# Kernel optimization log

Measured on AMD Instinct MI355X. Metric: run time of the kernel, lower is better.

The kernel has to match this reference:

```python
import jax, jax.numpy as jnp
import numpy as np

STEP_SIZE = 0.3333
MAX_STEPS = 8          # >= ceil(max(2*sigma)/step); extra iterations have k==0 (no-op)
TANGENT_DIRECTION = True


def _bilinear_sample(img, p):
    # img: [B,C,H,W], p: [B,2,H,W] normalized coords in [0,1] (x=width, y=height)
    B, C, H, W = img.shape
    fx = p[:, 0] * W - 0.5   # [B,H,W] pixel-center convention
    fy = p[:, 1] * H - 0.5
    x0 = jnp.floor(fx)
    y0 = jnp.floor(fy)
    wx = (fx - x0)[:, None]  # [B,1,H,W]
    wy = (fy - y0)[:, None]
    x0i = jnp.clip(x0.astype(jnp.int32), 0, W - 1)
    x1i = jnp.clip(x0i + 1, 0, W - 1)
    y0i = jnp.clip(y0.astype(jnp.int32), 0, H - 1)
    y1i = jnp.clip(y0i + 1, 0, H - 1)
    gather = jax.vmap(lambda im, yi, xi: im[:, yi, xi])  # per-batch gather -> [B,C,H,W]
    v00 = gather(img, y0i, x0i)
    v01 = gather(img, y0i, x1i)
    v10 = gather(img, y1i, x0i)
    v11 = gather(img, y1i, x1i)
    return (v00 * (1 - wx) + v01 * wx) * (1 - wy) + (v10 * (1 - wx) + v11 * wx) * wy


def _p_start(H, W, dtype):
    xs = (jnp.arange(W, dtype=dtype) + 0.5) / W
    ys = (jnp.arange(H, dtype=dtype) + 0.5) / H
    px = jnp.broadcast_to(xs[None, :], (H, W))
    py = jnp.broadcast_to(ys[:, None], (H, W))
    return jnp.stack([px, py])[None]  # [1,2,H,W]


def _perp(t):
    return jnp.concatenate([t[:, 1:2], -t[:, 0:1]], axis=1)


def _forward(x, tangent, sigma):
    B, C, H, W = x.shape
    dt = x.dtype
    factor = min(H, W) / 1024.0          # input_size_factor relative to 1024 base res
    sigma = sigma * factor               # [B,1,1,1]
    half_width = 2.0 * sigma
    two_sigma2 = 2.0 * sigma * sigma
    step = jnp.asarray(1.0 / (STEP_SIZE * factor), dtype=dt)
    tex = jnp.array([W, H], dtype=dt).reshape(1, 2, 1, 1)
    p0 = _p_start(H, W, dt)

    def one_pass(direction):
        v = direction if TANGENT_DIRECTION else _perp(direction)
        p = p0 + v / tex
        r = jnp.broadcast_to(step, (B, 1, 1, 1))
        c = jnp.zeros_like(x)
        s = jnp.zeros((B, 1, H, W), dt)

        def body(carry, _):
            c, s, v, p, r = carry
            k = jnp.exp(-r * r / two_sigma2)                 # [B,1,1,1]
            k = jnp.where(r < half_width, k, 0.0)
            inb = ((p[:, 0:1] >= 0.0) & (p[:, 0:1] < 1.0) &
                   (p[:, 1:2] >= 0.0) & (p[:, 1:2] < 1.0))   # [B,1,H,W]
            k = jnp.where(inb, k, 0.0)                        # [B,1,H,W]
            c = c + _bilinear_sample(x, p) * k
            s = s + k
            tf = _bilinear_sample(tangent, p)                 # [B,2,H,W]
            if not TANGENT_DIRECTION:
                tf = _perp(tf)
            vt = jnp.sum(v * tf, axis=1, keepdims=True)
            tf = jnp.where(vt < 0.0, -tf, tf)                 # keep marching direction coherent
            return (c, s, tf, p + tf / tex, r + step), None

        (c, s, _, _, _), _ = jax.lax.scan(body, (c, s, v, p, r), None, length=MAX_STEPS)
        return c, s

    c1, s1 = one_pass(tangent)
    c2, s2 = one_pass(-tangent)
    return (x + c1 + c2) / (1.0 + s1 + s2)


def setup_inputs() -> dict:
    key = jax.random.key(0)
    k1, k2, k3 = jax.random.split(key, 3)
    B, C, H, W = 2, 3, 1024, 1024
    x = jax.random.uniform(k1, (B, C, H, W), dtype=jnp.float32)
    t = jax.random.normal(k2, (B, 2, H, W), dtype=jnp.float32)
    t = t / (jnp.sqrt(jnp.sum(t * t, axis=1, keepdims=True)) + 1e-6)  # unit tangent field
    sigma = 2.0 + 4.0 * jax.random.uniform(k3, (B, 1, 1, 1), dtype=jnp.float32)
    return {"x": x, "tangent": t, "sigma": sigma}


def reference(x, tangent, sigma):
    return _forward(x, tangent, sigma)
```

## Files before the change

### kernel.cpp

```cpp
#include <hip/hip_runtime.h>


#define HH 1024
#define WW 1024
#define CC 3
#define BB 2
#define NPIX (HH * WW)

#define TSX 16
#define TSY 16
#define HALO_LO 4
#define NWIN 25

__device__ __forceinline__ unsigned bf16rn(float f) {
    unsigned u = __float_as_uint(f);
    return (u + 0x7fffu + ((u >> 16) & 1u)) >> 16;
}
__device__ __forceinline__ float bf_lo(unsigned u) { return __uint_as_float(u << 16); }
__device__ __forceinline__ float bf_hi(unsigned u) { return __uint_as_float(u & 0xffff0000u); }
__device__ __forceinline__ float uaf(unsigned u)   { return __uint_as_float(u); }

__global__ __launch_bounds__(256) void flow_smooth_lds(
    const float* __restrict__ x, const float* __restrict__ tng,
    const float* __restrict__ sigma, float* __restrict__ out)
{
    __shared__ uint4 win[NWIN * NWIN];

    const int id  = (int)blockIdx.x + ((int)blockIdx.y << 6) + ((int)blockIdx.z << 12);
    const int swz = ((id & 7) << 10) + (id >> 3);
    const int bx = swz & 63;
    const int by = (swz >> 6) & 63;
    const int b  = swz >> 12;

    const int tile_x0 = bx * TSX;
    const int tile_y0 = by * TSY;
    const int win_x0 = tile_x0 - HALO_LO;
    const int win_y0 = tile_y0 - HALO_LO;
    const bool border = (bx == 0) | (bx == 63) | (by == 0) | (by == 63);

    const float* __restrict__ xb  = x   + (size_t)b * CC * NPIX;
    const float* __restrict__ tbx = tng + (size_t)b * 2 * NPIX;
    const float* __restrict__ tby = tbx + NPIX;

    if (!border) {
        const int gbase = win_y0 * WW + win_x0;
        for (unsigned j = threadIdx.x; j < NWIN * NWIN; j += 256) {
            const int jy = (int)(j / NWIN);
            const int jx = (int)j - jy * NWIN;
            const int g = gbase + (jy << 10) + jx;
            uint4 rec;
            rec.x = __float_as_uint(tbx[g]);
            rec.y = __float_as_uint(tby[g]);
            rec.z = bf16rn(xb[g]) | (bf16rn(xb[NPIX + g]) << 16);
            rec.w = bf16rn(xb[2 * NPIX + g]);
            win[j] = rec;
        }
    } else {
        for (unsigned j = threadIdx.x; j < NWIN * NWIN; j += 256) {
            const int jy = (int)(j / NWIN);
            const int jx = (int)j - jy * NWIN;
            const int gy = min(max(win_y0 + jy, 0), HH - 1);
            const int gx = min(max(win_x0 + jx, 0), WW - 1);
            const int g = gy * WW + gx;
            uint4 rec;
            rec.x = __float_as_uint(tbx[g]);
            rec.y = __float_as_uint(tby[g]);
            rec.z = bf16rn(xb[g]) | (bf16rn(xb[NPIX + g]) << 16);
            rec.w = bf16rn(xb[2 * NPIX + g]);
            win[j] = rec;
        }
    }
    __syncthreads();

    const int tx = threadIdx.x & (TSX - 1);
    const int ty = threadIdx.x >> 4;
    const int ix = tile_x0 + tx;
    const int iy = tile_y0 + ty;
    const int pix = iy * WW + ix;

    const float sig = sigma[b];
    const float half_width = 2.0f * sig;
    const float inv2s2 = 1.0f / (2.0f * sig * sig);
    const float step = (float)(1.0 / 0.3333);

    const float r0 = step;
    const float r1 = r0 + step;
    const float r2 = r1 + step;
    const int nlive = (int)(r0 < half_width) + (int)(r1 < half_width) + (int)(r2 < half_width);
    float kk[3];
    kk[0] = __expf(-r0 * r0 * inv2s2);
    kk[1] = __expf(-r1 * r1 * inv2s2);
    kk[2] = __expf(-r2 * r2 * inv2s2);

    const float xc0 = xb[pix];
    const float xc1 = xb[NPIX + pix];
    const float xc2 = xb[2 * NPIX + pix];
    const int cidx = (ty + HALO_LO) * NWIN + (tx + HALO_LO);
    const uint2 qc = *reinterpret_cast<const uint2*>(&win[cidx]);
    const float t0x = uaf(qc.x);
    const float t0y = uaf(qc.y);

    const float invW = 1.0f / WW;
    const float invH = 1.0f / HH;

    float acc0 = 0.f, acc1 = 0.f, acc2 = 0.f, accs = 0.f;

    float vx[2], vy[2], px[2], py[2];
    vx[0] = t0x;  vy[0] = t0y;
    vx[1] = -t0x; vy[1] = -t0y;
    const float p0x = ((float)ix + 0.5f) * invW;
    const float p0y = ((float)iy + 0.5f) * invH;
    px[0] = p0x + vx[0] * invW;  py[0] = p0y + vy[0] * invH;
    px[1] = p0x + vx[1] * invW;  py[1] = p0y + vy[1] * invH;

    if (!border) {
        const int winoff = win_y0 * NWIN + win_x0;
        #pragma unroll
        for (int it = 0; it < 3; ++it) {
            if (it >= nlive) break;
            const float k = kk[it];
            #pragma unroll
            for (int c = 0; c < 2; ++c) {
                const float fx = fmaf(px[c], (float)WW, -0.5f);
                const float fy = fmaf(py[c], (float)HH, -0.5f);
                const float x0f = floorf(fx);
                const float y0f = floorf(fy);
                const float wx = fx - x0f;
                const float wy = fy - y0f;
                const int idx = (int)y0f * NWIN + (int)x0f - winoff;

                const uint4 q00 = win[idx];
                const uint4 q01 = win[idx + 1];
                const uint4 q10 = win[idx + NWIN];
                const uint4 q11 = win[idx + NWIN + 1];

                const float wxm = 1.f - wx, wym = 1.f - wy;
                const float w00 = wxm * wym, w01 = wx * wym;
                const float w10 = wxm * wy,  w11 = wx * wy;

                float tfx = uaf(q00.x) * w00 + uaf(q01.x) * w01
                          + uaf(q10.x) * w10 + uaf(q11.x) * w11;
                float tfy = uaf(q00.y) * w00 + uaf(q01.y) * w01
                          + uaf(q10.y) * w10 + uaf(q11.y) * w11;

                const float k00 = k * w00, k01 = k * w01;
                const float k10 = k * w10, k11 = k * w11;
                acc0 += bf_lo(q00.z) * k00 + bf_lo(q01.z) * k01
                      + bf_lo(q10.z) * k10 + bf_lo(q11.z) * k11;
                acc1 += bf_hi(q00.z) * k00 + bf_hi(q01.z) * k01
                      + bf_hi(q10.z) * k10 + bf_hi(q11.z) * k11;
                acc2 += bf_lo(q00.w) * k00 + bf_lo(q01.w) * k01
                      + bf_lo(q10.w) * k10 + bf_lo(q11.w) * k11;

                const float vt = vx[c] * tfx + vy[c] * tfy;
                const unsigned sgn = __float_as_uint(vt) & 0x80000000u;
                tfx = __uint_as_float(__float_as_uint(tfx) ^ sgn);
                tfy = __uint_as_float(__float_as_uint(tfy) ^ sgn);
                vx[c] = tfx; vy[c] = tfy;
                px[c] += tfx * invW;
                py[c] += tfy * invH;
            }
        }
        float ks = 0.f;
        if (nlive > 0) ks += kk[0];
        if (nlive > 1) ks += kk[1];
        if (nlive > 2) ks += kk[2];
        accs = 2.0f * ks;
    } else {
        #pragma unroll
        for (int it = 0; it < 3; ++it) {
            if (it >= nlive) break;
            const float k = kk[it];
            #pragma unroll
            for (int c = 0; c < 2; ++c) {
                const float fx = fmaf(px[c], (float)WW, -0.5f);
                const float fy = fmaf(py[c], (float)HH, -0.5f);
                const float x0f = floorf(fx);
                const float y0f = floorf(fy);
                const float wx = fx - x0f;
                const float wy = fy - y0f;
                int x0i = (int)x0f;
                int y0i = (int)y0f;
                x0i = min(max(x0i, 0), WW - 1);
                y0i = min(max(y0i, 0), HH - 1);
                const int x1i = min(x0i + 1, WW - 1);
                const int y1i = min(y0i + 1, HH - 1);

                const int jx0 = x0i - win_x0;
                const int jx1 = x1i - win_x0;
                const int jy0 = y0i - win_y0;
                const int jy1 = y1i - win_y0;

                const uint4 q00 = win[jy0 * NWIN + jx0];
                const uint4 q01 = win[jy0 * NWIN + jx1];
                const uint4 q10 = win[jy1 * NWIN + jx0];
                const uint4 q11 = win[jy1 * NWIN + jx1];

                const float wxm = 1.f - wx, wym = 1.f - wy;
                const float w00 = wxm * wym, w01 = wx * wym;
                const float w10 = wxm * wy,  w11 = wx * wy;

                float tfx = uaf(q00.x) * w00 + uaf(q01.x) * w01
                          + uaf(q10.x) * w10 + uaf(q11.x) * w11;
                float tfy = uaf(q00.y) * w00 + uaf(q01.y) * w01
                          + uaf(q10.y) * w10 + uaf(q11.y) * w11;

                const bool inb = (px[c] >= 0.f) & (px[c] < 1.f) &
                                 (py[c] >= 0.f) & (py[c] < 1.f);
                const float kg = inb ? k : 0.f;
                const float k00 = kg * w00, k01 = kg * w01;
                const float k10 = kg * w10, k11 = kg * w11;
                acc0 += bf_lo(q00.z) * k00 + bf_lo(q01.z) * k01
                      + bf_lo(q10.z) * k10 + bf_lo(q11.z) * k11;
                acc1 += bf_hi(q00.z) * k00 + bf_hi(q01.z) * k01
                      + bf_hi(q10.z) * k10 + bf_hi(q11.z) * k11;
                acc2 += bf_lo(q00.w) * k00 + bf_lo(q01.w) * k01
                      + bf_lo(q10.w) * k10 + bf_lo(q11.w) * k11;
                accs += kg;

                const float vt = vx[c] * tfx + vy[c] * tfy;
                const unsigned sgn = __float_as_uint(vt) & 0x80000000u;
                tfx = __uint_as_float(__float_as_uint(tfx) ^ sgn);
                tfy = __uint_as_float(__float_as_uint(tfy) ^ sgn);
                vx[c] = tfx; vy[c] = tfy;
                px[c] += tfx * invW;
                py[c] += tfy * invH;
            }
        }
    }

    const float inv_den = 1.0f / (1.0f + accs);
    float* ob = out + (size_t)b * CC * NPIX;
    ob[pix]            = (xc0 + acc0) * inv_den;
    ob[NPIX + pix]     = (xc1 + acc1) * inv_den;
    ob[2 * NPIX + pix] = (xc2 + acc2) * inv_den;
}

extern "C" void kernel_launch(void* const* d_in, const int* in_sizes, int n_in,
                              void* d_out, int out_size, void* d_ws, size_t ws_size,
                              hipStream_t stream) {
    const float* x  = (const float*)d_in[0];
    const float* t  = (const float*)d_in[1];
    const float* sg = (const float*)d_in[2];
    float* out = (float*)d_out;

    dim3 grid(WW / TSX, HH / TSY, BB);
    flow_smooth_lds<<<grid, dim3(256), 0, stream>>>(x, t, sg, out);
}
```

Measured before the change: 114.7 us.

## Split LDS window into tangent and fp16 color arrays, use packed half FMA

Splits the single 16-byte LDS record into a float2 tangent array and an 8-byte fp16 color array. Color interpolation now runs with packed half2 FMAs instead of bf16 unpacking and scalar FMAs. The tangent sample on the last live iteration is skipped, since its result is never used. Packed half arithmetic for the weighted sums adds rounding error compared to fp32 accumulation, and splitting the arrays means more LDS load instructions per tap.

```diff
diff --git a/kernel.cpp b/kernel.cpp
--- a/kernel.cpp
+++ b/kernel.cpp
@@ -1,4 +1,5 @@
 #include <hip/hip_runtime.h>
+#include <hip/hip_fp16.h>
 
 
 #define HH 1024
@@ -12,19 +13,17 @@
 #define HALO_LO 4
 #define NWIN 25
 
-__device__ __forceinline__ unsigned bf16rn(float f) {
-    unsigned u = __float_as_uint(f);
-    return (u + 0x7fffu + ((u >> 16) & 1u)) >> 16;
+__device__ __forceinline__ float uaf(unsigned u) { return __uint_as_float(u); }
+__device__ __forceinline__ __half2 h2(unsigned u) {
+    __half2 r; *(unsigned*)&r = u; return r;
 }
-__device__ __forceinline__ float bf_lo(unsigned u) { return __uint_as_float(u << 16); }
-__device__ __forceinline__ float bf_hi(unsigned u) { return __uint_as_float(u & 0xffff0000u); }
-__device__ __forceinline__ float uaf(unsigned u)   { return __uint_as_float(u); }
 
 __global__ __launch_bounds__(256) void flow_smooth_lds(
     const float* __restrict__ x, const float* __restrict__ tng,
     const float* __restrict__ sigma, float* __restrict__ out)
 {
-    __shared__ uint4 win[NWIN * NWIN];
+    __shared__ float2 tanw[NWIN * NWIN];
+    __shared__ uint2  colw[NWIN * NWIN];
 
     const int id  = (int)blockIdx.x + ((int)blockIdx.y << 6) + ((int)blockIdx.z << 12);
     const int swz = ((id & 7) << 10) + (id >> 3);
@@ -48,12 +47,13 @@
             const int jy = (int)(j / NWIN);
             const int jx = (int)j - jy * NWIN;
             const int g = gbase + (jy << 10) + jx;
-            uint4 rec;
-            rec.x = __float_as_uint(tbx[g]);
-            rec.y = __float_as_uint(tby[g]);
-            rec.z = bf16rn(xb[g]) | (bf16rn(xb[NPIX + g]) << 16);
-            rec.w = bf16rn(xb[2 * NPIX + g]);
-            win[j] = rec;
+            tanw[j] = make_float2(tbx[g], tby[g]);
+            const __half2 c01 = __floats2half2_rn(xb[g], xb[NPIX + g]);
+            const __half2 c2p = __floats2half2_rn(xb[2 * NPIX + g], 0.f);
+            uint2 r;
+            r.x = *(const unsigned*)&c01;
+            r.y = *(const unsigned*)&c2p;
+            colw[j] = r;
         }
     } else {
         for (unsigned j = threadIdx.x; j < NWIN * NWIN; j += 256) {
@@ -62,12 +62,13 @@
             const int gy = min(max(win_y0 + jy, 0), HH - 1);
             const int gx = min(max(win_x0 + jx, 0), WW - 1);
             const int g = gy * WW + gx;
-            uint4 rec;
-            rec.x = __float_as_uint(tbx[g]);
-            rec.y = __float_as_uint(tby[g]);
-            rec.z = bf16rn(xb[g]) | (bf16rn(xb[NPIX + g]) << 16);
-            rec.w = bf16rn(xb[2 * NPIX + g]);
-            win[j] = rec;
+            tanw[j] = make_float2(tbx[g], tby[g]);
+            const __half2 c01 = __floats2half2_rn(xb[g], xb[NPIX + g]);
+            const __half2 c2p = __floats2half2_rn(xb[2 * NPIX + g], 0.f);
+            uint2 r;
+            r.x = *(const unsigned*)&c01;
+            r.y = *(const unsigned*)&c2p;
+            colw[j] = r;
         }
     }
     __syncthreads();
@@ -87,18 +88,17 @@
     const float r1 = r0 + step;
     const float r2 = r1 + step;
     const int nlive = (int)(r0 < half_width) + (int)(r1 < half_width) + (int)(r2 < half_width);
-    float kk[3];
-    kk[0] = __expf(-r0 * r0 * inv2s2);
-    kk[1] = __expf(-r1 * r1 * inv2s2);
-    kk[2] = __expf(-r2 * r2 * inv2s2);
+    const float kk0 = __expf(-r0 * r0 * inv2s2);
+    const float kk1 = __expf(-r1 * r1 * inv2s2);
+    const float kk2 = __expf(-r2 * r2 * inv2s2);
 
     const float xc0 = xb[pix];
     const float xc1 = xb[NPIX + pix];
     const float xc2 = xb[2 * NPIX + pix];
     const int cidx = (ty + HALO_LO) * NWIN + (tx + HALO_LO);
-    const uint2 qc = *reinterpret_cast<const uint2*>(&win[cidx]);
-    const float t0x = uaf(qc.x);
-    const float t0y = uaf(qc.y);
+    const float2 tc = tanw[cidx];
+    const float t0x = tc.x;
+    const float t0y = tc.y;
 
     const float invW = 1.0f / WW;
     const float invH = 1.0f / HH;
@@ -118,7 +118,8 @@
         #pragma unroll
         for (int it = 0; it < 3; ++it) {
             if (it >= nlive) break;
-            const float k = kk[it];
+            const float k = (it == 0) ? kk0 : (it == 1) ? kk1 : kk2;
+            const bool need_t = (it + 1 < nlive);
             #pragma unroll
             for (int c = 0; c < 2; ++c) {
                 const float fx = fmaf(px[c], (float)WW, -0.5f);
@@ -129,48 +130,57 @@
                 const float wy = fy - y0f;
                 const int idx = (int)y0f * NWIN + (int)x0f - winoff;
 
-                const uint4 q00 = win[idx];
-                const uint4 q01 = win[idx + 1];
-                const uint4 q10 = win[idx + NWIN];
-                const uint4 q11 = win[idx + NWIN + 1];
-
                 const float wxm = 1.f - wx, wym = 1.f - wy;
                 const float w00 = wxm * wym, w01 = wx * wym;
                 const float w10 = wxm * wy,  w11 = wx * wy;
 
-                float tfx = uaf(q00.x) * w00 + uaf(q01.x) * w01
-                          + uaf(q10.x) * w10 + uaf(q11.x) * w11;
-                float tfy = uaf(q00.y) * w00 + uaf(q01.y) * w01
-                          + uaf(q10.y) * w10 + uaf(q11.y) * w11;
-
-                const float k00 = k * w00, k01 = k * w01;
-                const float k10 = k * w10, k11 = k * w11;
-                acc0 += bf_lo(q00.z) * k00 + bf_lo(q01.z) * k01
-                      + bf_lo(q10.z) * k10 + bf_lo(q11.z) * k11;
-                acc1 += bf_hi(q00.z) * k00 + bf_hi(q01.z) * k01
-                      + bf_hi(q10.z) * k10 + bf_hi(q11.z) * k11;
-                acc2 += bf_lo(q00.w) * k00 + bf_lo(q01.w) * k01
-                      + bf_lo(q10.w) * k10 + bf_lo(q11.w) * k11;
-
-                const float vt = vx[c] * tfx + vy[c] * tfy;
-                const unsigned sgn = __float_as_uint(vt) & 0x80000000u;
-                tfx = __uint_as_float(__float_as_uint(tfx) ^ sgn);
-                tfy = __uint_as_float(__float_as_uint(tfy) ^ sgn);
-                vx[c] = tfx; vy[c] = tfy;
-                px[c] += tfx * invW;
-                py[c] += tfy * invH;
+                const uint2 q00 = colw[idx];
+                const uint2 q01 = colw[idx + 1];
+                const uint2 q10 = colw[idx + NWIN];
+                const uint2 q11 = colw[idx + NWIN + 1];
+                const __half2 h00 = __float2half2_rn(w00);
+                const __half2 h01 = __float2half2_rn(w01);
+                const __half2 h10 = __float2half2_rn(w10);
+                const __half2 h11 = __float2half2_rn(w11);
+                __half2 a01 = __hmul2(h00, h2(q00.x));
+                a01 = __hfma2(h01, h2(q01.x), a01);
+                a01 = __hfma2(h10, h2(q10.x), a01);
+                a01 = __hfma2(h11, h2(q11.x), a01);
+                __half2 a2 = __hmul2(h00, h2(q00.y));
+                a2 = __hfma2(h01, h2(q01.y), a2);
+                a2 = __hfma2(h10, h2(q10.y), a2);
+                a2 = __hfma2(h11, h2(q11.y), a2);
+                acc0 = fmaf(k, __low2float(a01), acc0);
+                acc1 = fmaf(k, __high2float(a01), acc1);
+                acc2 = fmaf(k, __low2float(a2), acc2);
+
+                if (need_t) {
+                    const float2 t00 = tanw[idx];
+                    const float2 t01 = tanw[idx + 1];
+                    const float2 t10 = tanw[idx + NWIN];
+                    const float2 t11 = tanw[idx + NWIN + 1];
+                    float tfx = t00.x * w00 + t01.x * w01 + t10.x * w10 + t11.x * w11;
+                    float tfy = t00.y * w00 + t01.y * w01 + t10.y * w10 + t11.y * w11;
+                    const float vt = vx[c] * tfx + vy[c] * tfy;
+                    const unsigned sgn = __float_as_uint(vt) & 0x80000000u;
+                    tfx = __uint_as_float(__float_as_uint(tfx) ^ sgn);
+                    tfy = __uint_as_float(__float_as_uint(tfy) ^ sgn);
+                    vx[c] = tfx; vy[c] = tfy;
+                    px[c] += tfx * invW;
+                    py[c] += tfy * invH;
+                }
             }
         }
         float ks = 0.f;
-        if (nlive > 0) ks += kk[0];
-        if (nlive > 1) ks += kk[1];
-        if (nlive > 2) ks += kk[2];
+        if (nlive > 0) ks += kk0;
+        if (nlive > 1) ks += kk1;
+        if (nlive > 2) ks += kk2;
         accs = 2.0f * ks;
     } else {
         #pragma unroll
         for (int it = 0; it < 3; ++it) {
             if (it >= nlive) break;
-            const float k = kk[it];
+            const float k = (it == 0) ? kk0 : (it == 1) ? kk1 : kk2;
             #pragma unroll
             for (int c = 0; c < 2; ++c) {
                 const float fx = fmaf(px[c], (float)WW, -0.5f);
@@ -190,34 +200,46 @@
                 const int jx1 = x1i - win_x0;
                 const int jy0 = y0i - win_y0;
                 const int jy1 = y1i - win_y0;
-
-                const uint4 q00 = win[jy0 * NWIN + jx0];
-                const uint4 q01 = win[jy0 * NWIN + jx1];
-                const uint4 q10 = win[jy1 * NWIN + jx0];
-                const uint4 q11 = win[jy1 * NWIN + jx1];
+                const int i00 = jy0 * NWIN + jx0;
+                const int i01 = jy0 * NWIN + jx1;
+                const int i10 = jy1 * NWIN + jx0;
+                const int i11 = jy1 * NWIN + jx1;
 
                 const float wxm = 1.f - wx, wym = 1.f - wy;
                 const float w00 = wxm * wym, w01 = wx * wym;
                 const float w10 = wxm * wy,  w11 = wx * wy;
 
-                float tfx = uaf(q00.x) * w00 + uaf(q01.x) * w01
-                          + uaf(q10.x) * w10 + uaf(q11.x) * w11;
-                float tfy = uaf(q00.y) * w00 + uaf(q01.y) * w01
-                          + uaf(q10.y) * w10 + uaf(q11.y) * w11;
-
                 const bool inb = (px[c] >= 0.f) & (px[c] < 1.f) &
                                  (py[c] >= 0.f) & (py[c] < 1.f);
                 const float kg = inb ? k : 0.f;
-                const float k00 = kg * w00, k01 = kg * w01;
-                const float k10 = kg * w10, k11 = kg * w11;
-                acc0 += bf_lo(q00.z) * k00 + bf_lo(q01.z) * k01
-                      + bf_lo(q10.z) * k10 + bf_lo(q11.z) * k11;
-                acc1 += bf_hi(q00.z) * k00 + bf_hi(q01.z) * k01
-                      + bf_hi(q10.z) * k10 + bf_hi(q11.z) * k11;
-                acc2 += bf_lo(q00.w) * k00 + bf_lo(q01.w) * k01
-                      + bf_lo(q10.w) * k10 + bf_lo(q11.w) * k11;
+
+                const uint2 q00 = colw[i00];
+                const uint2 q01 = colw[i01];
+                const uint2 q10 = colw[i10];
+                const uint2 q11 = colw[i11];
+                const __half2 h00 = __float2half2_rn(w00);
+                const __half2 h01 = __float2half2_rn(w01);
+                const __half2 h10 = __float2half2_rn(w10);
+                const __half2 h11 = __float2half2_rn(w11);
+                __half2 a01 = __hmul2(h00, h2(q00.x));
+                a01 = __hfma2(h01, h2(q01.x), a01);
+                a01 = __hfma2(h10, h2(q10.x), a01);
+                a01 = __hfma2(h11, h2(q11.x), a01);
+                __half2 a2 = __hmul2(h00, h2(q00.y));
+                a2 = __hfma2(h01, h2(q01.y), a2);
+                a2 = __hfma2(h10, h2(q10.y), a2);
+                a2 = __hfma2(h11, h2(q11.y), a2);
+                acc0 = fmaf(kg, __low2float(a01), acc0);
+                acc1 = fmaf(kg, __high2float(a01), acc1);
+                acc2 = fmaf(kg, __low2float(a2), acc2);
                 accs += kg;
 
+                const float2 t00 = tanw[i00];
+                const float2 t01 = tanw[i01];
+                const float2 t10 = tanw[i10];
+                const float2 t11 = tanw[i11];
+                float tfx = t00.x * w00 + t01.x * w01 + t10.x * w10 + t11.x * w11;
+                float tfy = t00.y * w00 + t01.y * w01 + t10.y * w10 + t11.y * w11;
                 const float vt = vx[c] * tfx + vy[c] * tfy;
                 const unsigned sgn = __float_as_uint(vt) & 0x80000000u;
                 tfx = __uint_as_float(__float_as_uint(tfx) ^ sgn);
```

Measured after the change: 108.4 us. -5.5%, faster.
